# Kernel optimization log

Measured on AMD Instinct MI355X. Metric: run time of the kernel, lower is better.

## Reference

```python
import jax, jax.numpy as jnp
import numpy as np

B, T, H = 2048, 10, 512
IN1, IN2 = 16, 15  # encoder input_size / input_size1 (hardcoded in source)


def lstm_step(x, h, c, Wih, Whh, bih, bhh):
    # torch nn.LSTM gate order: i, f, g, o
    g = x @ Wih.T + h @ Whh.T + bih + bhh
    i, f, gg, o = jnp.split(g, 4, axis=-1)
    c_new = jax.nn.sigmoid(f) * c + jax.nn.sigmoid(i) * jnp.tanh(gg)
    h_new = jax.nn.sigmoid(o) * jnp.tanh(c_new)
    return h_new, c_new


def setup_inputs() -> dict:
    key = jax.random.key(0)
    ks = jax.random.split(key, 24)
    def rn(k, shape, scale=0.05):
        return jax.random.normal(k, shape, dtype=jnp.float32) * scale
    return {
        "X": jax.random.normal(ks[0], (B, T - 1, IN2), dtype=jnp.float32),
        "y_prev": jax.random.normal(ks[1], (B, T - 1), dtype=jnp.float32),
        # encoder attention: Linear(2H + T - 1, 1)
        "enc_attn_W": rn(ks[2], (1, 2 * H + T - 1)),
        "enc_attn_b": rn(ks[3], (1,)),
        # encoder LSTM (input 16, hidden H)
        "enc_lstm_Wih": rn(ks[4], (4 * H, IN1)),
        "enc_lstm_Whh": rn(ks[5], (4 * H, H)),
        "enc_lstm_bih": rn(ks[6], (4 * H,)),
        "enc_lstm_bhh": rn(ks[7], (4 * H,)),
        # encoder LSTM1 (input 15, hidden H)
        "enc_lstm1_Wih": rn(ks[8], (4 * H, IN2)),
        "enc_lstm1_Whh": rn(ks[9], (4 * H, H)),
        "enc_lstm1_bih": rn(ks[10], (4 * H,)),
        "enc_lstm1_bhh": rn(ks[11], (4 * H,)),
        # decoder attn_layer: Linear(6H, H) -> Linear(H, 1)  (no nonlinearity)
        "dec_attn1_W": rn(ks[12], (H, 6 * H)),
        "dec_attn1_b": rn(ks[13], (H,)),
        "dec_attn2_W": rn(ks[14], (1, H)),
        "dec_attn2_b": rn(ks[15], (1,)),
        # decoder LSTM (input 1, hidden 2H)
        "dec_lstm_Wih": rn(ks[16], (8 * H, 1)),
        "dec_lstm_Whh": rn(ks[17], (8 * H, 2 * H)),
        "dec_lstm_bih": rn(ks[18], (8 * H,)),
        "dec_lstm_bhh": rn(ks[19], (8 * H,)),
        # fc: Linear(2H + 1, 1)  (weight.data.normal_() -> scale 1)
        "fc_W": rn(ks[20], (1, 2 * H + 1), 1.0),
        "fc_b": rn(ks[21], (1,)),
        # fc_final: Linear(4H, 1)
        "fc_final_W": rn(ks[22], (1, 4 * H)),
        "fc_final_b": rn(ks[23], (1,)),
    }


def reference(X, y_prev, enc_attn_W, enc_attn_b,
              enc_lstm_Wih, enc_lstm_Whh, enc_lstm_bih, enc_lstm_bhh,
              enc_lstm1_Wih, enc_lstm1_Whh, enc_lstm1_bih, enc_lstm1_bhh,
              dec_attn1_W, dec_attn1_b, dec_attn2_W, dec_attn2_b,
              dec_lstm_Wih, dec_lstm_Whh, dec_lstm_bih, dec_lstm_bhh,
              fc_W, fc_b, fc_final_W, fc_final_b):
    Bn = X.shape[0]
    # ---------------- Encoder ----------------
    x_y = jnp.concatenate([X, y_prev[..., None]], axis=2)      # (B, T-1, 16)
    mm = X * y_prev[..., None]                                  # (B, T-1, 15)
    # attention weight split: [h | s | features-over-time]
    Wh = enc_attn_W[0, :H]
    Ws = enc_attn_W[0, H:2 * H]
    Wf = enc_attn_W[0, 2 * H:]
    # per-driving-series time profile term, constant over loop steps
    base1 = jnp.swapaxes(x_y, 1, 2) @ Wf + enc_attn_b[0]        # (B, 16)
    base2 = jnp.swapaxes(mm, 1, 2) @ Wf + enc_attn_b[0]         # (B, 15)

    def enc_step(carry, xs):
        h1, s1, h2, s2 = carry
        xy_t, mm_t = xs                                          # (B,16),(B,15)
        sc1 = base1 + (h1 @ Wh + s1 @ Ws)[:, None]               # (B, 16)
        a1 = jax.nn.softmax(sc1, axis=1)
        x_tilde = a1 * xy_t
        h1, s1 = lstm_step(x_tilde, h1, s1, enc_lstm_Wih, enc_lstm_Whh,
                           enc_lstm_bih, enc_lstm_bhh)
        sc2 = base2 + (h2 @ Wh + s2 @ Ws)[:, None]               # (B, 15)
        a2 = jax.nn.softmax(sc2, axis=1)
        x_tilde1 = a2 * mm_t
        h2, s2 = lstm_step(x_tilde1, h2, s2, enc_lstm1_Wih, enc_lstm1_Whh,
                           enc_lstm1_bih, enc_lstm1_bhh)
        return (h1, s1, h2, s2), jnp.concatenate([h1, h2], axis=1)

    z = jnp.zeros((Bn, H), jnp.float32)
    _, enc_hs = jax.lax.scan(enc_step, (z, z, z, z),
                             (jnp.swapaxes(x_y, 0, 1), jnp.swapaxes(mm, 0, 1)))
    X_encoded = jnp.swapaxes(enc_hs, 0, 1)                       # (B, T-1, 2H)

    # ---------------- Decoder ----------------
    W1d = dec_attn1_W[:, :2 * H]      # (H, 2H) for d_n
    W1c = dec_attn1_W[:, 2 * H:4 * H]  # (H, 2H) for c_n
    W1x = dec_attn1_W[:, 4 * H:]      # (H, 2H) for X_encoded
    hx = jnp.einsum('btd,hd->bth', X_encoded, W1x)               # (B, T-1, H)

    def dec_step(carry, y_t):
        d, c = carry                                             # (B, 2H)
        hid = hx + (d @ W1d.T + c @ W1c.T)[:, None, :] + dec_attn1_b
        score = hid @ dec_attn2_W[0] + dec_attn2_b[0]            # (B, T-1)
        beta = jax.nn.softmax(score, axis=1)
        context = jnp.einsum('bt,btd->bd', beta, X_encoded)      # (B, 2H)
        y_tilde = jnp.concatenate([context, y_t[:, None]], axis=1) @ fc_W.T + fc_b
        d, c = lstm_step(y_tilde, d, c, dec_lstm_Wih, dec_lstm_Whh,
                         dec_lstm_bih, dec_lstm_bhh)
        return (d, c), context

    z2 = jnp.zeros((Bn, 2 * H), jnp.float32)
    (d, _), ctxs = jax.lax.scan(dec_step, (z2, z2), jnp.swapaxes(y_prev, 0, 1))
    context = ctxs[-1]  # context of last step (computed before the final LSTM update)
    y_pred = jnp.concatenate([d, context], axis=1) @ fc_final_W.T + fc_final_b
    return y_pred  # (B, 1)
```

## Files before the change

kernel.cpp:

```cpp
#include <hip/hip_runtime.h>
#include <hip/hip_bf16.h>
#include <math.h>

#define Bsz 2048
#define T1  9
#define Hs  512
#define IN2 15

typedef __bf16 bf16x8 __attribute__((ext_vector_type(8)));
typedef float  f32x4  __attribute__((ext_vector_type(4)));
typedef __hip_bfloat16 bf16;


#define BMT 128
#define BNP 128

struct GA {
  const bf16* Ahi;
  const bf16* Axhi;
  const bf16* Whi;
  const float* bsum;
  const float* wihp;
  const float* ytp;
  float* c;
  bf16* Hhi;
  float* hf;
  int hf_stride;
  int ytstride;
};

template<int HG, int KPAD, bool HAS_X, int ZD>
__global__ __launch_bounds__(256, 2)
void lstm2_k(GA a0, GA a1) {
  constexpr int KT = KPAD / 32;
  constexpr int GX = (4 * HG) / BNP;
  constexpr int GY = Bsz / BMT;
  constexpr int NWG = GX * GY * ZD;
  constexpr int Q = NWG / 8;

  __shared__ __align__(16) unsigned short As[2][BMT * 32];
  __shared__ __align__(16) unsigned short Bh[2][BNP * 32];

  const int tid = threadIdx.x;
  const int orig = blockIdx.x + GX * (blockIdx.y + GY * blockIdx.z);
  const int swz = (orig & 7) * Q + (orig >> 3);
  const bool sel = (ZD == 2) && (swz >= GX * GY);
  const bf16* __restrict__ Ahi  = sel ? a1.Ahi  : a0.Ahi;
  const bf16* __restrict__ Axhi = sel ? a1.Axhi : a0.Axhi;
  const bf16* __restrict__ Whi  = sel ? a1.Whi  : a0.Whi;
  const float* __restrict__ bsum = sel ? a1.bsum : a0.bsum;
  const float* __restrict__ wihp = sel ? a1.wihp : a0.wihp;
  const float* __restrict__ ytp  = sel ? a1.ytp  : a0.ytp;
  float* __restrict__ cst = sel ? a1.c   : a0.c;
  bf16*  __restrict__ Hhi = sel ? a1.Hhi : a0.Hhi;
  float* __restrict__ hf  = sel ? a1.hf  : a0.hf;
  const int hf_stride = sel ? a1.hf_stride : a0.hf_stride;
  const int ytstride  = sel ? a1.ytstride  : a0.ytstride;

  const int rem = (ZD == 2) ? (swz & (GX * GY - 1)) : swz;
  const int nb = rem / GY;
  const int mb = rem % GY;
  const int m0 = mb * BMT, n0 = nb * BNP;

  const int kcb = (tid & 3) * 8;
  const int ra = tid >> 2;

  uint4 s0, s1, s2, s5;
  auto stage_load = [&](int kt) {
    const int ke = kt * 32 + kcb;
    if (!HAS_X || ke < HG) {
      const size_t ag = (size_t)(m0 + ra) * HG + ke;
      s0 = *reinterpret_cast<const uint4*>(Ahi + ag);
      s5 = *reinterpret_cast<const uint4*>(Ahi + ag + (size_t)64 * HG);
    } else if (ke < HG + 16) {
      s0 = *reinterpret_cast<const uint4*>(Axhi + (size_t)(m0 + ra) * 16 + (ke - HG));
      s5 = *reinterpret_cast<const uint4*>(Axhi + (size_t)(m0 + ra + 64) * 16 + (ke - HG));
    } else {
      s0.x = s0.y = s0.z = s0.w = 0u;
      s5 = s0;
    }
    const size_t bg = (size_t)(n0 + ra) * KPAD + ke;
    s1 = *reinterpret_cast<const uint4*>(Whi + bg);
    s2 = *reinterpret_cast<const uint4*>(Whi + bg + (size_t)64 * KPAD);
  };
  const int wofA = (ra * 32 + kcb) ^ ((ra & 7) << 3);
  const int wofB = wofA + 64 * 32;
  auto stage_write = [&](int p) {
    *reinterpret_cast<uint4*>(&As[p][wofA]) = s0;
    *reinterpret_cast<uint4*>(&As[p][wofB]) = s5;
    *reinterpret_cast<uint4*>(&Bh[p][wofA]) = s1;
    *reinterpret_cast<uint4*>(&Bh[p][wofB]) = s2;
  };

  const int lane = tid & 63;
  const int wv = tid >> 6;
  const int wr = wv >> 1, wc = wv & 1;
  const int l15 = lane & 15;
  const int lk = (lane >> 4) * 8;

  const int rswz = (l15 & 7) << 3;
  const int aoff0 = (((wr * 64 + l15) * 32) + lk) ^ rswz;
  const int boff0 = (((wc * 64 + l15) * 32) + lk) ^ rswz;

  f32x4 acc[4][4] = {};

  stage_load(0);
  stage_write(0);
  stage_load(1);

  for (int kt = 0; kt < KT; ++kt) {
    __syncthreads();
    if (kt + 1 < KT) stage_write((kt + 1) & 1);
    const int p = kt & 1;

    bf16x8 ah[4];
#pragma unroll
    for (int mi = 0; mi < 4; ++mi)
      ah[mi] = __builtin_bit_cast(bf16x8,
                 *reinterpret_cast<const uint4*>(&As[p][aoff0 + mi * 512]));
    if (kt + 2 < KT) stage_load(kt + 2);
#pragma unroll
    for (int ni = 0; ni < 4; ++ni) {
      bf16x8 bhv = __builtin_bit_cast(bf16x8,
                     *reinterpret_cast<const uint4*>(&Bh[p][boff0 + ni * 512]));
#pragma unroll
      for (int mi = 0; mi < 4; ++mi)
        acc[mi][ni] = __builtin_amdgcn_mfma_f32_16x16x32_bf16(ah[mi], bhv, acc[mi][ni], 0, 0, 0);
    }
  }

  const int j = nb * 32 + wc * 16 + l15;
  const int npb = nb * 128 + wc * 64 + l15;
  const float bs0 = bsum[npb], bs1 = bsum[npb + 16];
  const float bs2 = bsum[npb + 32], bs3 = bsum[npb + 48];
  float w0 = 0.f, w1 = 0.f, w2 = 0.f, w3 = 0.f;
  if (!HAS_X) {
    w0 = wihp[npb]; w1 = wihp[npb + 16];
    w2 = wihp[npb + 32]; w3 = wihp[npb + 48];
  }
#pragma unroll
  for (int mi = 0; mi < 4; ++mi) {
#pragma unroll
    for (int r = 0; r < 4; ++r) {
      const int rowl = wr * 64 + mi * 16 + (lane >> 4) * 4 + r;
      const size_t rowg = m0 + rowl;
      float gi = acc[mi][0][r] + bs0;
      float gf = acc[mi][1][r] + bs1;
      float gg = acc[mi][2][r] + bs2;
      float go = acc[mi][3][r] + bs3;
      if (!HAS_X) {
        const float yv = ytp[rowg * ytstride];
        gi += yv * w0; gf += yv * w1; gg += yv * w2; go += yv * w3;
      }
      const float i_ = 1.f / (1.f + __expf(-gi));
      const float f_ = 1.f / (1.f + __expf(-gf));
      const float tg = __expf(2.f * gg);
      const float g_ = (tg - 1.f) / (tg + 1.f);
      const float o_ = 1.f / (1.f + __expf(-go));
      const size_t idx = rowg * HG + j;
      const float cn = f_ * cst[idx] + i_ * g_;
      cst[idx] = cn;
      const float tc = __expf(2.f * cn);
      const float hn = o_ * (tc - 1.f) / (tc + 1.f);
      Hhi[idx] = __float2bfloat16(hn);
      if (hf) hf[rowg * hf_stride + j] = hn;
    }
  }
}

__global__ void build_all_w_k(
    const float* __restrict__ W0hh, const float* __restrict__ W0ih,
    const float* __restrict__ b0ih, const float* __restrict__ b0hh,
    const float* __restrict__ W1hh, const float* __restrict__ W1ih,
    const float* __restrict__ b1ih, const float* __restrict__ b1hh,
    const float* __restrict__ Wdhh, const float* __restrict__ Wdih,
    const float* __restrict__ bdih, const float* __restrict__ bdhh,
    bf16* __restrict__ W0hi, bf16* __restrict__ W1hi, bf16* __restrict__ Wdhi,
    float* __restrict__ bs0, float* __restrict__ bs1,
    float* __restrict__ bsd, float* __restrict__ wihp) {
  const int bid = blockIdx.x;
  const float *Whh, *Wih, *bih, *bhh;
  bf16 *Whi;
  float *bsum, *wp;
  int HG, nx, Kpad, base;
  if (bid < 544) {
    Whh = W0hh; Wih = W0ih; bih = b0ih; bhh = b0hh;
    Whi = W0hi; bsum = bs0; wp = nullptr;
    HG = Hs; nx = 16; Kpad = 544; base = 0;
  } else if (bid < 1088) {
    Whh = W1hh; Wih = W1ih; bih = b1ih; bhh = b1hh;
    Whi = W1hi; bsum = bs1; wp = nullptr;
    HG = Hs; nx = 15; Kpad = 544; base = 544;
  } else {
    Whh = Wdhh; Wih = Wdih; bih = bdih; bhh = bdhh;
    Whi = Wdhi; bsum = bsd; wp = wihp;
    HG = 2 * Hs; nx = 0; Kpad = 1024; base = 1088;
  }
  const int chunks = Kpad >> 3;
  const int idx = (bid - base) * 256 + threadIdx.x;
  if (idx >= 4 * HG * chunks) return;
  const int np = idx / chunks;
  const int k0 = (idx - np * chunks) << 3;
  const int g = (np >> 4) & 3;
  const int jj = ((np >> 6) << 4) + (np & 15);
  const int norig = g * HG + jj;
  float v[8];
  if (k0 + 8 <= HG) {
    const float4* s = reinterpret_cast<const float4*>(Whh + (size_t)norig * HG + k0);
    float4 v0 = s[0], v1 = s[1];
    v[0] = v0.x; v[1] = v0.y; v[2] = v0.z; v[3] = v0.w;
    v[4] = v1.x; v[5] = v1.y; v[6] = v1.z; v[7] = v1.w;
  } else {
#pragma unroll
    for (int u = 0; u < 8; ++u) {
      const int k = k0 + u;
      v[u] = (k < HG) ? Whh[(size_t)norig * HG + k]
                      : ((k - HG < nx) ? Wih[(size_t)norig * nx + (k - HG)] : 0.f);
    }
  }
  unsigned short hh[8];
#pragma unroll
  for (int u = 0; u < 8; ++u) {
    const bf16 h = __float2bfloat16(v[u]);
    hh[u] = *reinterpret_cast<const unsigned short*>(&h);
  }
  const size_t off = (size_t)np * Kpad + k0;
  *reinterpret_cast<uint4*>((unsigned short*)Whi + off) = *reinterpret_cast<uint4*>(hh);
  if (k0 == 0) {
    bsum[np] = bih[norig] + bhh[norig];
    if (wp) wp[np] = Wih[norig];
  }
}

__global__ void prep_attn_k(const float* __restrict__ X, const float* __restrict__ yp,
                            const float* __restrict__ encW, const float* __restrict__ encb,
                            bf16* __restrict__ x1h, bf16* __restrict__ x2h) {
  const int b = blockIdx.x;
  const int tid = threadIdx.x;
  __shared__ float wf[T1], ypb[T1];
  __shared__ float s1[16], s2[IN2], e1[16], e2[IN2];
  if (tid < T1) {
    wf[tid] = encW[2 * Hs + tid];
    ypb[tid] = yp[(size_t)b * T1 + tid];
  }
  __syncthreads();
  const float bb = encb[0];
  if (tid < 16) {
    float acc = bb;
    for (int t = 0; t < T1; ++t) {
      float xv = (tid < IN2) ? X[(size_t)b * (T1 * IN2) + t * IN2 + tid] : ypb[t];
      acc += xv * wf[t];
    }
    s1[tid] = acc;
  } else if (tid < 16 + IN2) {
    const int k = tid - 16;
    float acc = bb;
    for (int t = 0; t < T1; ++t)
      acc += X[(size_t)b * (T1 * IN2) + t * IN2 + k] * ypb[t] * wf[t];
    s2[k] = acc;
  }
  __syncthreads();
  if (tid < 16) {
    float m = -1e30f;
    for (int k = 0; k < 16; ++k) m = fmaxf(m, s1[k]);
    e1[tid] = expf(s1[tid] - m);
  } else if (tid < 16 + IN2) {
    const int k = tid - 16;
    float m = -1e30f;
    for (int kk = 0; kk < IN2; ++kk) m = fmaxf(m, s2[kk]);
    e2[k] = expf(s2[k] - m);
  }
  __syncthreads();
  if (tid < 16) {
    float sum = 0.f;
    for (int k = 0; k < 16; ++k) sum += e1[k];
    const float a = e1[tid] / sum;
    for (int t = 0; t < T1; ++t) {
      float xv = (tid < IN2) ? X[(size_t)b * (T1 * IN2) + t * IN2 + tid] : ypb[t];
      x1h[((size_t)t * Bsz + b) * 16 + tid] = __float2bfloat16(a * xv);
    }
  } else if (tid < 16 + IN2) {
    const int k = tid - 16;
    float sum = 0.f;
    for (int kk = 0; kk < IN2; ++kk) sum += e2[kk];
    const float a = e2[k] / sum;
    for (int t = 0; t < T1; ++t)
      x2h[((size_t)t * Bsz + b) * 16 + k] =
          __float2bfloat16(a * X[(size_t)b * (T1 * IN2) + t * IN2 + k] * ypb[t]);
  } else if (tid == 31) {
    const bf16 z = __float2bfloat16(0.f);
    for (int t = 0; t < T1; ++t) x2h[((size_t)t * Bsz + b) * 16 + 15] = z;
  }
}

__global__ void prep_v_k(const float* __restrict__ A1W, const float* __restrict__ A2W,
                         float* __restrict__ v) {
  const int dd = blockIdx.x;
  const int l = threadIdx.x;
  float acc = 0.f;
#pragma unroll
  for (int k = 0; k < 8; ++k) {
    const int h = l + 64 * k;
    acc += A2W[h] * A1W[(size_t)h * (6 * Hs) + 4 * Hs + dd];
  }
#pragma unroll
  for (int off = 32; off > 0; off >>= 1) acc += __shfl_down(acc, off);
  if (l == 0) v[dd] = acc;
}

__global__ void dec_ctx_k(const float* __restrict__ Xe, const float* __restrict__ v,
                          const float* __restrict__ yp, const float* __restrict__ fcW,
                          const float* __restrict__ fcb,
                          float* __restrict__ ctx, float* __restrict__ yt) {
  const int b = blockIdx.x;
  const int tid = threadIdx.x;
  const int lane = tid & 63, wid = tid >> 6;
  const float* xb = Xe + (size_t)b * (T1 * 2 * Hs);
  const int d0 = tid * 4;
  const float4 v4 = *reinterpret_cast<const float4*>(v + d0);
  float4 x4[T1];
  float s[T1];
#pragma unroll
  for (int t = 0; t < T1; ++t) {
    x4[t] = *reinterpret_cast<const float4*>(xb + t * 2 * Hs + d0);
    s[t] = x4[t].x * v4.x + x4[t].y * v4.y + x4[t].z * v4.z + x4[t].w * v4.w;
  }
  __shared__ float part[T1][4];
  __shared__ float score[T1];
  __shared__ float tot2[4];
  __shared__ float cfs;
#pragma unroll
  for (int t = 0; t < T1; ++t) {
    float r = s[t];
#pragma unroll
    for (int off = 32; off > 0; off >>= 1) r += __shfl_down(r, off);
    if (lane == 0) part[t][wid] = r;
  }
  __syncthreads();
  if (tid < T1) score[tid] = part[tid][0] + part[tid][1] + part[tid][2] + part[tid][3];
  __syncthreads();
  float mx = -1e30f;
#pragma unroll
  for (int t = 0; t < T1; ++t) mx = fmaxf(mx, score[t]);
  float e[T1];
  float sum = 0.f;
#pragma unroll
  for (int t = 0; t < T1; ++t) { e[t] = expf(score[t] - mx); sum += e[t]; }
  const float inv = 1.f / sum;
  float4 c4 = {0.f, 0.f, 0.f, 0.f};
#pragma unroll
  for (int t = 0; t < T1; ++t) {
    c4.x += e[t] * x4[t].x; c4.y += e[t] * x4[t].y;
    c4.z += e[t] * x4[t].z; c4.w += e[t] * x4[t].w;
  }
  c4.x *= inv; c4.y *= inv; c4.z *= inv; c4.w *= inv;
  *reinterpret_cast<float4*>(ctx + (size_t)b * 2 * Hs + d0) = c4;
  const float4 f4 = *reinterpret_cast<const float4*>(fcW + d0);
  float fcacc = c4.x * f4.x + c4.y * f4.y + c4.z * f4.z + c4.w * f4.w;
#pragma unroll
  for (int off = 32; off > 0; off >>= 1) fcacc += __shfl_down(fcacc, off);
  if (lane == 0) tot2[wid] = fcacc;
  __syncthreads();
  if (tid == 0) cfs = tot2[0] + tot2[1] + tot2[2] + tot2[3] + fcb[0];
  __syncthreads();
  if (tid < T1) yt[(size_t)b * T1 + tid] = cfs + yp[(size_t)b * T1 + tid] * fcW[2 * Hs];
}

__global__ void final_out_k(const float* __restrict__ dfin, const float* __restrict__ ctx,
                            const float* __restrict__ Wfin, const float* __restrict__ bfin,
                            float* __restrict__ out) {
  const int b = blockIdx.x;
  const int tid = threadIdx.x;
  const int lane = tid & 63, wid = tid >> 6;
  const int d0 = tid * 4;
  const float4 a4 = *reinterpret_cast<const float4*>(dfin + (size_t)b * 2 * Hs + d0);
  const float4 w4 = *reinterpret_cast<const float4*>(Wfin + d0);
  const float4 c4 = *reinterpret_cast<const float4*>(ctx + (size_t)b * 2 * Hs + d0);
  const float4 u4 = *reinterpret_cast<const float4*>(Wfin + 2 * Hs + d0);
  float acc = a4.x * w4.x + a4.y * w4.y + a4.z * w4.z + a4.w * w4.w
            + c4.x * u4.x + c4.y * u4.y + c4.z * u4.z + c4.w * u4.w;
#pragma unroll
  for (int off = 32; off > 0; off >>= 1) acc += __shfl_down(acc, off);
  __shared__ float red[4];
  if (lane == 0) red[wid] = acc;
  __syncthreads();
  if (tid == 0) out[b] = red[0] + red[1] + red[2] + red[3] + bfin[0];
}

extern "C" void kernel_launch(void* const* d_in, const int* in_sizes, int n_in,
                              void* d_out, int out_size, void* d_ws, size_t ws_size,
                              hipStream_t stream) {
  const float* X     = (const float*)d_in[0];
  const float* yp    = (const float*)d_in[1];
  const float* encW  = (const float*)d_in[2];
  const float* encb  = (const float*)d_in[3];
  const float* e0Wih = (const float*)d_in[4];
  const float* e0Whh = (const float*)d_in[5];
  const float* e0bih = (const float*)d_in[6];
  const float* e0bhh = (const float*)d_in[7];
  const float* e1Wih = (const float*)d_in[8];
  const float* e1Whh = (const float*)d_in[9];
  const float* e1bih = (const float*)d_in[10];
  const float* e1bhh = (const float*)d_in[11];
  const float* dA1W  = (const float*)d_in[12];
  const float* dA2W  = (const float*)d_in[14];
  const float* dWih  = (const float*)d_in[16];
  const float* dWhh  = (const float*)d_in[17];
  const float* dbih  = (const float*)d_in[18];
  const float* dbhh  = (const float*)d_in[19];
  const float* fcW   = (const float*)d_in[20];
  const float* fcb   = (const float*)d_in[21];
  const float* WfinW = (const float*)d_in[22];
  const float* Wfinb = (const float*)d_in[23];
  float* out = (float*)d_out;
  (void)in_sizes; (void)n_in; (void)out_size; (void)ws_size;

  char* wsb = (char*)d_ws;
  size_t off = 0;
  auto alloc = [&](size_t bytes) -> void* {
    void* p = wsb + off;
    off = (off + bytes + 255) & ~(size_t)255;
    return p;
  };
  const size_t BH  = (size_t)Bsz * Hs;
  const size_t BH2 = (size_t)Bsz * 2 * Hs;
  float* c1   = (float*)alloc(BH * 4);
  float* c2   = (float*)alloc(BH * 4);
  float* cdec = (float*)alloc(BH2 * 4);
  bf16* h1hi0 = (bf16*)alloc(BH * 2);
  bf16* h2hi0 = (bf16*)alloc(BH * 2);
  bf16* dhi0  = (bf16*)alloc(BH2 * 2);
  const size_t zero_bytes = off;
  bf16* h1hi1 = (bf16*)alloc(BH * 2);
  bf16* h2hi1 = (bf16*)alloc(BH * 2);
  bf16* dhi1  = (bf16*)alloc(BH2 * 2);
  bf16* W0hi  = (bf16*)alloc((size_t)2048 * 544 * 2);
  bf16* W1hi  = (bf16*)alloc((size_t)2048 * 544 * 2);
  bf16* Wdhi  = (bf16*)alloc((size_t)4096 * 1024 * 2);
  float* bs0  = (float*)alloc(2048 * 4);
  float* bs1  = (float*)alloc(2048 * 4);
  float* bsd  = (float*)alloc(4096 * 4);
  float* wihp = (float*)alloc(4096 * 4);
  bf16* x1h   = (bf16*)alloc((size_t)T1 * Bsz * 16 * 2);
  bf16* x2h   = (bf16*)alloc((size_t)T1 * Bsz * 16 * 2);
  float* Xe   = (float*)alloc((size_t)Bsz * T1 * 2 * Hs * 4);
  float* dfp  = (float*)alloc(BH2 * 4);
  float* ctx  = (float*)alloc(BH2 * 4);
  float* vv   = (float*)alloc(2 * Hs * 4);
  float* yt   = (float*)alloc((size_t)Bsz * T1 * 4);

  hipMemsetAsync(d_ws, 0, zero_bytes, stream);

  build_all_w_k<<<3136, 256, 0, stream>>>(
      e0Whh, e0Wih, e0bih, e0bhh, e1Whh, e1Wih, e1bih, e1bhh,
      dWhh, dWih, dbih, dbhh,
      W0hi, W1hi, Wdhi, bs0, bs1, bsd, wihp);
  prep_attn_k<<<Bsz, 64, 0, stream>>>(X, yp, encW, encb, x1h, x2h);
  prep_v_k<<<2 * Hs, 64, 0, stream>>>(dA1W, dA2W, vv);

  bf16 *h1c = h1hi0, *h1n = h1hi1;
  bf16 *h2c = h2hi0, *h2n = h2hi1;
  for (int t = 0; t < T1; ++t) {
    GA a0{h1c, x1h + (size_t)t * Bsz * 16, W0hi, bs0, nullptr, nullptr,
          c1, h1n, Xe + (size_t)t * 2 * Hs, T1 * 2 * Hs, 0};
    GA a1{h2c, x2h + (size_t)t * Bsz * 16, W1hi, bs1, nullptr, nullptr,
          c2, h2n, Xe + (size_t)t * 2 * Hs + Hs, T1 * 2 * Hs, 0};
    dim3 grid((4 * Hs) / BNP, Bsz / BMT, 2);
    lstm2_k<Hs, 544, true, 2><<<grid, 256, 0, stream>>>(a0, a1);
    bf16* tp;
    tp = h1c; h1c = h1n; h1n = tp;
    tp = h2c; h2c = h2n; h2n = tp;
  }

  dec_ctx_k<<<Bsz, 256, 0, stream>>>(Xe, vv, yp, fcW, fcb, ctx, yt);

  bf16 *dc = dhi0, *dn = dhi1;
  for (int t = 0; t < T1; ++t) {
    GA a0{dc, nullptr, Wdhi, bsd, wihp, yt + t,
          cdec, dn, (t == T1 - 1) ? dfp : nullptr, 2 * Hs, T1};
    dim3 grid((8 * Hs) / BNP, Bsz / BMT, 1);
    lstm2_k<2 * Hs, 1024, false, 1><<<grid, 256, 0, stream>>>(a0, a0);
    bf16* tp = dc; dc = dn; dn = tp;
  }

  final_out_k<<<Bsz, 256, 0, stream>>>(dfp, ctx, WfinW, Wfinb, out);
}
```

Measured before the change: 538.2 us.

## Split K across two wavegroups per block with LDS reduction in LSTM GEMM

Doubles the LSTM GEMM block to 512 threads. Two 256-thread groups each process half of the K dimension into separate LDS buffers, and group 1's accumulators are then reduced into group 0 through shared memory before the epilogue. The encoder K padding grows from 544 to 576 so that K splits evenly into 64-wide steps, and the weight-build grid is resized to match. The aim is more waves per block to hide latency in this small-grid, latency-bound recurrent GEMM. The cost is an extra LDS reduction, twice the shared memory, and more padded zero work on the encoder.

Result: slower. 614.4 us (+14.2%).

```diff
diff --git a/kernel.cpp b/kernel.cpp
--- a/kernel.cpp
+++ b/kernel.cpp
@@ -30,16 +30,16 @@
 };
 
 template<int HG, int KPAD, bool HAS_X, int ZD>
-__global__ __launch_bounds__(256, 2)
+__global__ __launch_bounds__(512, 2)
 void lstm2_k(GA a0, GA a1) {
-  constexpr int KT = KPAD / 32;
+  constexpr int KT2 = KPAD / 64;
   constexpr int GX = (4 * HG) / BNP;
   constexpr int GY = Bsz / BMT;
   constexpr int NWG = GX * GY * ZD;
   constexpr int Q = NWG / 8;
 
-  __shared__ __align__(16) unsigned short As[2][BMT * 32];
-  __shared__ __align__(16) unsigned short Bh[2][BNP * 32];
+  __shared__ __align__(16) unsigned short As[2][2][4096];
+  __shared__ __align__(16) unsigned short Bh[2][2][4096];
 
   const int tid = threadIdx.x;
   const int orig = blockIdx.x + GX * (blockIdx.y + GY * blockIdx.z);
@@ -62,12 +62,14 @@
   const int mb = rem % GY;
   const int m0 = mb * BMT, n0 = nb * BNP;
 
-  const int kcb = (tid & 3) * 8;
-  const int ra = tid >> 2;
+  const int tl = tid & 255;
+  const int grp = tid >> 8;
+  const int kcb = (tl & 3) * 8;
+  const int ra = tl >> 2;
 
   uint4 s0, s1, s2, s5;
-  auto stage_load = [&](int kt) {
-    const int ke = kt * 32 + kcb;
+  auto stage_load = [&](int ktt) {
+    const int ke = (ktt + grp * KT2) * 32 + kcb;
     if (!HAS_X || ke < HG) {
       const size_t ag = (size_t)(m0 + ra) * HG + ke;
       s0 = *reinterpret_cast<const uint4*>(Ahi + ag);
@@ -84,17 +86,18 @@
     s2 = *reinterpret_cast<const uint4*>(Whi + bg + (size_t)64 * KPAD);
   };
   const int wofA = (ra * 32 + kcb) ^ ((ra & 7) << 3);
-  const int wofB = wofA + 64 * 32;
+  const int wofB = wofA + 2048;
   auto stage_write = [&](int p) {
-    *reinterpret_cast<uint4*>(&As[p][wofA]) = s0;
-    *reinterpret_cast<uint4*>(&As[p][wofB]) = s5;
-    *reinterpret_cast<uint4*>(&Bh[p][wofA]) = s1;
-    *reinterpret_cast<uint4*>(&Bh[p][wofB]) = s2;
+    *reinterpret_cast<uint4*>(&As[p][grp][wofA]) = s0;
+    *reinterpret_cast<uint4*>(&As[p][grp][wofB]) = s5;
+    *reinterpret_cast<uint4*>(&Bh[p][grp][wofA]) = s1;
+    *reinterpret_cast<uint4*>(&Bh[p][grp][wofB]) = s2;
   };
 
   const int lane = tid & 63;
   const int wv = tid >> 6;
-  const int wr = wv >> 1, wc = wv & 1;
+  const int wl = wv & 3;
+  const int wr = wl >> 1, wc = wl & 1;
   const int l15 = lane & 15;
   const int lk = (lane >> 4) * 8;
 
@@ -108,26 +111,50 @@
   stage_write(0);
   stage_load(1);
 
-  for (int kt = 0; kt < KT; ++kt) {
+  for (int kt = 0; kt < KT2; ++kt) {
     __syncthreads();
-    if (kt + 1 < KT) stage_write((kt + 1) & 1);
+    if (kt + 1 < KT2) stage_write((kt + 1) & 1);
     const int p = kt & 1;
 
     bf16x8 ah[4];
 #pragma unroll
     for (int mi = 0; mi < 4; ++mi)
       ah[mi] = __builtin_bit_cast(bf16x8,
-                 *reinterpret_cast<const uint4*>(&As[p][aoff0 + mi * 512]));
-    if (kt + 2 < KT) stage_load(kt + 2);
+                 *reinterpret_cast<const uint4*>(&As[p][grp][aoff0 + mi * 512]));
+    if (kt + 2 < KT2) stage_load(kt + 2);
 #pragma unroll
     for (int ni = 0; ni < 4; ++ni) {
       bf16x8 bhv = __builtin_bit_cast(bf16x8,
-                     *reinterpret_cast<const uint4*>(&Bh[p][boff0 + ni * 512]));
+                     *reinterpret_cast<const uint4*>(&Bh[p][grp][boff0 + ni * 512]));
 #pragma unroll
       for (int mi = 0; mi < 4; ++mi)
         acc[mi][ni] = __builtin_amdgcn_mfma_f32_16x16x32_bf16(ah[mi], bhv, acc[mi][ni], 0, 0, 0);
     }
   }
+
+  __syncthreads();
+  {
+    float* region = (wl < 2) ? reinterpret_cast<float*>(&As[0][0][0]) + wl * 4096
+                             : reinterpret_cast<float*>(&Bh[0][0][0]) + (wl - 2) * 4096;
+    if (grp == 1) {
+#pragma unroll
+      for (int mi = 0; mi < 4; ++mi)
+#pragma unroll
+        for (int ni = 0; ni < 4; ++ni)
+          *reinterpret_cast<f32x4*>(region + (mi * 4 + ni) * 256 + lane * 4) = acc[mi][ni];
+    }
+    __syncthreads();
+    if (grp == 0) {
+#pragma unroll
+      for (int mi = 0; mi < 4; ++mi)
+#pragma unroll
+        for (int ni = 0; ni < 4; ++ni) {
+          f32x4 o = *reinterpret_cast<const f32x4*>(region + (mi * 4 + ni) * 256 + lane * 4);
+          acc[mi][ni] += o;
+        }
+    }
+  }
+  if (grp != 0) return;
 
   const int j = nb * 32 + wc * 16 + l15;
   const int npb = nb * 128 + wc * 64 + l15;
@@ -183,18 +210,18 @@
   bf16 *Whi;
   float *bsum, *wp;
   int HG, nx, Kpad, base;
-  if (bid < 544) {
+  if (bid < 576) {
     Whh = W0hh; Wih = W0ih; bih = b0ih; bhh = b0hh;
     Whi = W0hi; bsum = bs0; wp = nullptr;
-    HG = Hs; nx = 16; Kpad = 544; base = 0;
-  } else if (bid < 1088) {
+    HG = Hs; nx = 16; Kpad = 576; base = 0;
+  } else if (bid < 1152) {
     Whh = W1hh; Wih = W1ih; bih = b1ih; bhh = b1hh;
     Whi = W1hi; bsum = bs1; wp = nullptr;
-    HG = Hs; nx = 15; Kpad = 544; base = 544;
+    HG = Hs; nx = 15; Kpad = 576; base = 576;
   } else {
     Whh = Wdhh; Wih = Wdih; bih = bdih; bhh = bdhh;
     Whi = Wdhi; bsum = bsd; wp = wihp;
-    HG = 2 * Hs; nx = 0; Kpad = 1024; base = 1088;
+    HG = 2 * Hs; nx = 0; Kpad = 1024; base = 1152;
   }
   const int chunks = Kpad >> 3;
   const int idx = (bid - base) * 256 + threadIdx.x;
@@ -434,8 +461,8 @@
   bf16* h1hi1 = (bf16*)alloc(BH * 2);
   bf16* h2hi1 = (bf16*)alloc(BH * 2);
   bf16* dhi1  = (bf16*)alloc(BH2 * 2);
-  bf16* W0hi  = (bf16*)alloc((size_t)2048 * 544 * 2);
-  bf16* W1hi  = (bf16*)alloc((size_t)2048 * 544 * 2);
+  bf16* W0hi  = (bf16*)alloc((size_t)2048 * 576 * 2);
+  bf16* W1hi  = (bf16*)alloc((size_t)2048 * 576 * 2);
   bf16* Wdhi  = (bf16*)alloc((size_t)4096 * 1024 * 2);
   float* bs0  = (float*)alloc(2048 * 4);
   float* bs1  = (float*)alloc(2048 * 4);
@@ -451,7 +478,7 @@
 
   hipMemsetAsync(d_ws, 0, zero_bytes, stream);
 
-  build_all_w_k<<<3136, 256, 0, stream>>>(
+  build_all_w_k<<<3200, 256, 0, stream>>>(
       e0Whh, e0Wih, e0bih, e0bhh, e1Whh, e1Wih, e1bih, e1bhh,
       dWhh, dWih, dbih, dbhh,
       W0hi, W1hi, Wdhi, bs0, bs1, bsd, wihp);
@@ -466,7 +493,7 @@
     GA a1{h2c, x2h + (size_t)t * Bsz * 16, W1hi, bs1, nullptr, nullptr,
           c2, h2n, Xe + (size_t)t * 2 * Hs + Hs, T1 * 2 * Hs, 0};
     dim3 grid((4 * Hs) / BNP, Bsz / BMT, 2);
-    lstm2_k<Hs, 544, true, 2><<<grid, 256, 0, stream>>>(a0, a1);
+    lstm2_k<Hs, 576, true, 2><<<grid, 512, 0, stream>>>(a0, a1);
     bf16* tp;
     tp = h1c; h1c = h1n; h1n = tp;
     tp = h2c; h2c = h2n; h2n = tp;
@@ -479,7 +506,7 @@
     GA a0{dc, nullptr, Wdhi, bsd, wihp, yt + t,
           cdec, dn, (t == T1 - 1) ? dfp : nullptr, 2 * Hs, T1};
     dim3 grid((8 * Hs) / BNP, Bsz / BMT, 1);
-    lstm2_k<2 * Hs, 1024, false, 1><<<grid, 256, 0, stream>>>(a0, a0);
+    lstm2_k<2 * Hs, 1024, false, 1><<<grid, 512, 0, stream>>>(a0, a0);
     bf16* tp = dc; dc = dn; dn = tp;
   }
 
```

## Load GEMM tiles directly into LDS with global_load_lds and pad inputs

Applied to the files above, without the earlier changes.

Replaces the register-staged global-to-LDS copy in the LSTM GEMM kernel with direct global_load_lds instructions. Each lane's source address is permuted so the data lands in the XOR-swizzled LDS layout. The attention-weighted input buffers are widened from 16 to 32 columns, zero-padded, so every K tile can be fetched with the same direct load. This removes VGPR staging and the separate LDS write step, but keeps a single-stage prefetch per iteration, needs extra padding writes, and relies on the swizzle decode being correct.

After: 537.9 us. About the same (-0.1%).

```diff
diff --git a/kernel.cpp b/kernel.cpp
--- a/kernel.cpp
+++ b/kernel.cpp
@@ -10,6 +10,9 @@
 typedef __bf16 bf16x8 __attribute__((ext_vector_type(8)));
 typedef float  f32x4  __attribute__((ext_vector_type(4)));
 typedef __hip_bfloat16 bf16;
+
+#define AS1C const __attribute__((address_space(1))) void*
+#define AS3P __attribute__((address_space(3))) void*
 
 
 #define BMT 128
@@ -38,8 +41,8 @@
   constexpr int NWG = GX * GY * ZD;
   constexpr int Q = NWG / 8;
 
-  __shared__ __align__(16) unsigned short As[2][BMT * 32];
-  __shared__ __align__(16) unsigned short Bh[2][BNP * 32];
+  __shared__ __align__(16) unsigned short As[2][4096];
+  __shared__ __align__(16) unsigned short Bh[2][4096];
 
   const int tid = threadIdx.x;
   const int orig = blockIdx.x + GX * (blockIdx.y + GY * blockIdx.z);
@@ -62,39 +65,44 @@
   const int mb = rem % GY;
   const int m0 = mb * BMT, n0 = nb * BNP;
 
-  const int kcb = (tid & 3) * 8;
-  const int ra = tid >> 2;
-
-  uint4 s0, s1, s2, s5;
-  auto stage_load = [&](int kt) {
-    const int ke = kt * 32 + kcb;
-    if (!HAS_X || ke < HG) {
-      const size_t ag = (size_t)(m0 + ra) * HG + ke;
-      s0 = *reinterpret_cast<const uint4*>(Ahi + ag);
-      s5 = *reinterpret_cast<const uint4*>(Ahi + ag + (size_t)64 * HG);
-    } else if (ke < HG + 16) {
-      s0 = *reinterpret_cast<const uint4*>(Axhi + (size_t)(m0 + ra) * 16 + (ke - HG));
-      s5 = *reinterpret_cast<const uint4*>(Axhi + (size_t)(m0 + ra + 64) * 16 + (ke - HG));
-    } else {
-      s0.x = s0.y = s0.z = s0.w = 0u;
-      s5 = s0;
-    }
-    const size_t bg = (size_t)(n0 + ra) * KPAD + ke;
-    s1 = *reinterpret_cast<const uint4*>(Whi + bg);
-    s2 = *reinterpret_cast<const uint4*>(Whi + bg + (size_t)64 * KPAD);
-  };
-  const int wofA = (ra * 32 + kcb) ^ ((ra & 7) << 3);
-  const int wofB = wofA + 64 * 32;
-  auto stage_write = [&](int p) {
-    *reinterpret_cast<uint4*>(&As[p][wofA]) = s0;
-    *reinterpret_cast<uint4*>(&As[p][wofB]) = s5;
-    *reinterpret_cast<uint4*>(&Bh[p][wofA]) = s1;
-    *reinterpret_cast<uint4*>(&Bh[p][wofB]) = s2;
-  };
-
   const int lane = tid & 63;
   const int wv = tid >> 6;
-  const int wr = wv >> 1, wc = wv & 1;
+
+  auto dec_q = [](int q, int& row, int& col) {
+    const int hi = q >> 8;
+    const int qp = q & 255;
+    const int c2 = ((qp >> 2) ^ (qp >> 4)) & 1;
+    const int c1 = ((qp >> 1) ^ (qp >> 3)) & 1;
+    const int c0 = (qp ^ c2) & 1;
+    const int c = (qp & 0xF8) | (c2 << 2) | (c1 << 1) | c0;
+    row = hi * 64 + (c >> 2);
+    col = (c & 3) * 8;
+  };
+  int r0, c0, r1, c1;
+  dec_q(wv * 64 + lane, r0, c0);
+  dec_q((wv + 4) * 64 + lane, r1, c1);
+  const int ldsS0 = wv * 512;
+  const int ldsS1 = (wv + 4) * 512;
+
+  auto issue_tile = [&](int kt, int p) {
+    const int kb = kt * 32;
+    const bf16 *a0p, *a1p;
+    if (!HAS_X || kb < HG) {
+      a0p = Ahi + (size_t)(m0 + r0) * HG + kb + c0;
+      a1p = Ahi + (size_t)(m0 + r1) * HG + kb + c1;
+    } else {
+      a0p = Axhi + (size_t)(m0 + r0) * 32 + (kb - HG) + c0;
+      a1p = Axhi + (size_t)(m0 + r1) * 32 + (kb - HG) + c1;
+    }
+    const bf16* b0p = Whi + (size_t)(n0 + r0) * KPAD + kb + c0;
+    const bf16* b1p = Whi + (size_t)(n0 + r1) * KPAD + kb + c1;
+    __builtin_amdgcn_global_load_lds((AS1C)a0p, (AS3P)&As[p][ldsS0], 16, 0, 0);
+    __builtin_amdgcn_global_load_lds((AS1C)a1p, (AS3P)&As[p][ldsS1], 16, 0, 0);
+    __builtin_amdgcn_global_load_lds((AS1C)b0p, (AS3P)&Bh[p][ldsS0], 16, 0, 0);
+    __builtin_amdgcn_global_load_lds((AS1C)b1p, (AS3P)&Bh[p][ldsS1], 16, 0, 0);
+  };
+
+  const int wr = (wv >> 1), wc = wv & 1;
   const int l15 = lane & 15;
   const int lk = (lane >> 4) * 8;
 
@@ -104,21 +112,17 @@
 
   f32x4 acc[4][4] = {};
 
-  stage_load(0);
-  stage_write(0);
-  stage_load(1);
-
+  issue_tile(0, 0);
   for (int kt = 0; kt < KT; ++kt) {
     __syncthreads();
-    if (kt + 1 < KT) stage_write((kt + 1) & 1);
     const int p = kt & 1;
+    if (kt + 1 < KT) issue_tile(kt + 1, p ^ 1);
 
     bf16x8 ah[4];
 #pragma unroll
     for (int mi = 0; mi < 4; ++mi)
       ah[mi] = __builtin_bit_cast(bf16x8,
                  *reinterpret_cast<const uint4*>(&As[p][aoff0 + mi * 512]));
-    if (kt + 2 < KT) stage_load(kt + 2);
 #pragma unroll
     for (int ni = 0; ni < 4; ++ni) {
       bf16x8 bhv = __builtin_bit_cast(bf16x8,
@@ -277,7 +281,7 @@
     const float a = e1[tid] / sum;
     for (int t = 0; t < T1; ++t) {
       float xv = (tid < IN2) ? X[(size_t)b * (T1 * IN2) + t * IN2 + tid] : ypb[t];
-      x1h[((size_t)t * Bsz + b) * 16 + tid] = __float2bfloat16(a * xv);
+      x1h[((size_t)t * Bsz + b) * 32 + tid] = __float2bfloat16(a * xv);
     }
   } else if (tid < 16 + IN2) {
     const int k = tid - 16;
@@ -285,11 +289,18 @@
     for (int kk = 0; kk < IN2; ++kk) sum += e2[kk];
     const float a = e2[k] / sum;
     for (int t = 0; t < T1; ++t)
-      x2h[((size_t)t * Bsz + b) * 16 + k] =
+      x2h[((size_t)t * Bsz + b) * 32 + k] =
           __float2bfloat16(a * X[(size_t)b * (T1 * IN2) + t * IN2 + k] * ypb[t]);
   } else if (tid == 31) {
     const bf16 z = __float2bfloat16(0.f);
-    for (int t = 0; t < T1; ++t) x2h[((size_t)t * Bsz + b) * 16 + 15] = z;
+    for (int t = 0; t < T1; ++t) x2h[((size_t)t * Bsz + b) * 32 + 15] = z;
+  } else if (tid >= 32 && tid < 48) {
+    const int col = tid - 16;
+    const bf16 z = __float2bfloat16(0.f);
+    for (int t = 0; t < T1; ++t) {
+      x1h[((size_t)t * Bsz + b) * 32 + col] = z;
+      x2h[((size_t)t * Bsz + b) * 32 + col] = z;
+    }
   }
 }
 
@@ -441,8 +452,8 @@
   float* bs1  = (float*)alloc(2048 * 4);
   float* bsd  = (float*)alloc(4096 * 4);
   float* wihp = (float*)alloc(4096 * 4);
-  bf16* x1h   = (bf16*)alloc((size_t)T1 * Bsz * 16 * 2);
-  bf16* x2h   = (bf16*)alloc((size_t)T1 * Bsz * 16 * 2);
+  bf16* x1h   = (bf16*)alloc((size_t)T1 * Bsz * 32 * 2);
+  bf16* x2h   = (bf16*)alloc((size_t)T1 * Bsz * 32 * 2);
   float* Xe   = (float*)alloc((size_t)Bsz * T1 * 2 * Hs * 4);
   float* dfp  = (float*)alloc(BH2 * 4);
   float* ctx  = (float*)alloc(BH2 * 4);
@@ -461,9 +472,9 @@
   bf16 *h1c = h1hi0, *h1n = h1hi1;
   bf16 *h2c = h2hi0, *h2n = h2hi1;
   for (int t = 0; t < T1; ++t) {
-    GA a0{h1c, x1h + (size_t)t * Bsz * 16, W0hi, bs0, nullptr, nullptr,
+    GA a0{h1c, x1h + (size_t)t * Bsz * 32, W0hi, bs0, nullptr, nullptr,
           c1, h1n, Xe + (size_t)t * 2 * Hs, T1 * 2 * Hs, 0};
-    GA a1{h2c, x2h + (size_t)t * Bsz * 16, W1hi, bs1, nullptr, nullptr,
+    GA a1{h2c, x2h + (size_t)t * Bsz * 32, W1hi, bs1, nullptr, nullptr,
           c2, h2n, Xe + (size_t)t * 2 * Hs + Hs, T1 * 2 * Hs, 0};
     dim3 grid((4 * Hs) / BNP, Bsz / BMT, 2);
     lstm2_k<Hs, 544, true, 2><<<grid, 256, 0, stream>>>(a0, a1);
```
